# Optimization experiments

Hardware: AMD Instinct MI355X
Metric: run time of the kernel (lower is better)

## Reference

```python
import jax, jax.numpy as jnp
import numpy as np

B, S, D = 4, 1024, 1024
H, DK, DV = 16, 64, 64


def setup_inputs() -> dict:
    key = jax.random.key(0)
    ks = jax.random.split(key, 8)
    sc = 0.02
    return {
        "queries": jax.random.normal(ks[0], (B, S, D), jnp.float32),
        "keys": jax.random.normal(ks[1], (B, S, D), jnp.float32),
        "values": jax.random.normal(ks[2], (B, S, D), jnp.float32),
        "attn_bias": jax.random.normal(ks[3], (B, 1, S, S), jnp.float32),
        "Wq": jax.random.normal(ks[4], (H * DK, D), jnp.float32) * sc,
        "Wk": jax.random.normal(ks[5], (H * DK, D), jnp.float32) * sc,
        "Wv": jax.random.normal(ks[6], (H * DV, D), jnp.float32) * sc,
        "Wp": jax.random.normal(ks[7], (D, H * DV), jnp.float32) * sc,
    }


def reference(queries, keys, values, attn_bias, Wq, Wk, Wv, Wp):
    # Linear (no bias): x @ W.T, then split heads -> [B, H, S, d]
    q = (queries @ Wq.T).reshape(B, S, H, DK).transpose(0, 2, 1, 3)
    k = (keys @ Wk.T).reshape(B, S, H, DK).transpose(0, 2, 1, 3)
    v = (values @ Wv.T).reshape(B, S, H, DV).transpose(0, 2, 1, 3)
    # NOTE: original scales by d_model**-0.5, not d_key**-0.5
    scores = jnp.einsum("bhqd,bhkd->bhqk", q, k) * (D ** -0.5)
    scores = scores + attn_bias  # bias broadcasts over heads
    weights = jax.nn.softmax(scores, axis=-1)
    out = jnp.einsum("bhqk,bhkd->bhqd", weights, v)  # [B,H,S,DV]
    out = out.transpose(0, 2, 1, 3).reshape(B, S, H * DV)
    return out @ Wp.T
```

## Files before the change

kernel.cpp:

```cpp
#include <hip/hip_runtime.h>
#include <hip/hip_bf16.h>

typedef unsigned short u16;
typedef unsigned int u32;
typedef __attribute__((ext_vector_type(8))) short bf16x8;
typedef __attribute__((ext_vector_type(8))) u16 u16x8;
typedef __attribute__((ext_vector_type(4))) u16 u16x4;
typedef __attribute__((ext_vector_type(4))) u32 u32x4;
typedef __attribute__((ext_vector_type(4))) float f32x4;
typedef __attribute__((ext_vector_type(4))) _Float16 f16x4;
typedef __attribute__((ext_vector_type(8))) _Float16 f16x8;
typedef __attribute__((ext_vector_type(16))) float f32x16;

typedef const __attribute__((address_space(1))) void* gas1_t;
typedef __attribute__((address_space(3))) void* las3_t;

#define MFMA16(a,b,c) __builtin_amdgcn_mfma_f32_16x16x32_bf16((a),(b),(c),0,0,0)
#define MFMA32(a,b,c) __builtin_amdgcn_mfma_f32_32x32x16_bf16((a),(b),(c),0,0,0)

static constexpr int BB = 4, SS = 1024, DD = 1024, HH = 16;

static __device__ __forceinline__ u16 f2b(float x) {
  union { __hip_bfloat16 h; u16 u; } cv;
  cv.h = __float2bfloat16(x);
  return cv.u;
}
static __device__ __forceinline__ u32 pk2(float a, float b) {
  return (u32)f2b(a) | ((u32)f2b(b) << 16);
}
static __device__ __forceinline__ u32 cvtpk(float lo, float hi) {
  u32 r;
  asm("v_cvt_pk_bf16_f32 %0, %1, %2" : "=v"(r) : "v"(lo), "v"(hi));
  return r;
}

__global__ __launch_bounds__(256) void cvt_all(
    const float* __restrict__ wq_, const float* __restrict__ wk_, const float* __restrict__ wv_,
    const float* __restrict__ wp_, const float* __restrict__ bias,
    u16* __restrict__ wqb, u16* __restrict__ wkb, u16* __restrict__ wvb, u16* __restrict__ wpb,
    _Float16* __restrict__ bias16) {
  int bid = blockIdx.x;
  if (bid >= 4096) {
    int G = (bid - 4096) * 256 + threadIdx.x;
    int gi = G & 1023;
    int ctid = gi & 255, g = gi >> 8;
    int T = G >> 10;
    int kt = T & 15, qt = (T >> 4) & 7, b_ = T >> 7;
    int wq = ctid >> 6, hi = (ctid >> 5) & 1, ln = ctid & 31;
    int qrow = qt * 128 + wq * 32 + ln;
    int kbf = g >> 1, j = g & 1;
    int k0 = kt * 64 + kbf * 32 + j * 16 + hi * 4;
    const float* src = bias + (((size_t)(b_ * 1024 + qrow)) << 10) + k0;
    float4 lo = *(const float4*)(src);
    float4 up = *(const float4*)(src + 8);
    f16x8 r = { (_Float16)lo.x, (_Float16)lo.y, (_Float16)lo.z, (_Float16)lo.w,
                (_Float16)up.x, (_Float16)up.y, (_Float16)up.z, (_Float16)up.w };
    *(f16x8*)(bias16 + (((size_t)T) << 13) + g * 2048 + ctid * 8) = r;
    return;
  }
  const float* s; u16* d; int off;
  if      (bid < 1024) { s = wq_; d = wqb; off = bid; }
  else if (bid < 2048) { s = wk_; d = wkb; off = bid - 1024; }
  else if (bid < 3072) { s = wv_; d = wvb; off = bid - 2048; }
  else                 { s = wp_; d = wpb; off = bid - 3072; }
  int i = (off * 256 + threadIdx.x) * 4;
  float4 val = *(const float4*)(s + i);
  u16x4 r = { f2b(val.x), f2b(val.y), f2b(val.z), f2b(val.w) };
  *(u16x4*)(d + i) = r;
}

__global__ __launch_bounds__(512) void gemm_qkv(
    const float* __restrict__ Qf, const float* __restrict__ Kf, const float* __restrict__ Vf,
    const u16* __restrict__ Wbase, u16* __restrict__ Qb, u16* __restrict__ Kb,
    u16* __restrict__ Vtb) {
  const int z = blockIdx.z;
  const float* A = z == 0 ? Qf : (z == 1 ? Kf : Vf);
  const u16* W = Wbase + (size_t)z * (DD * DD);

  __shared__ __align__(16) float Af[128 * 64];
  __shared__ __align__(16) u16 Bs[128 * 64];

  const int tid = threadIdx.x;
  const int lane = tid & 63;
  const int wid = tid >> 6;
  const int g = lane >> 4;
  const int li = lane & 15;

  const int hw = blockIdx.x + (blockIdx.y << 3);
  const int L = ((hw & 7) << 5) + (hw >> 3);
  const int brow = (L >> 3) * 128;
  const int bcol = (L & 7) * 128;

  const int wr = (wid >> 1) * 32;
  const int wc = (wid & 1) * 64;

  const int arow = tid >> 4;
  const int apc = (tid & 15) ^ (arow & 15);
  const float* ga0 = A + (size_t)(brow + arow) * DD + apc * 4;

  const int srw = tid >> 3;
  const int spw = (tid & 7) ^ (srw & 7);
  const u16* gw0 = W + (size_t)(bcol + srw) * DD + spw * 8;

  f32x4 acc[2][4] = {};

  for (int k0 = 0; k0 < DD; k0 += 64) {
#pragma unroll
    for (int i = 0; i < 4; ++i)
      __builtin_amdgcn_global_load_lds((gas1_t)(const void*)(ga0 + (size_t)(i * 32) * DD + k0),
                                       (las3_t)(void*)(Af + (i * 32 + (wid << 2)) * 64), 16, 0, 0);
#pragma unroll
    for (int i = 0; i < 2; ++i)
      __builtin_amdgcn_global_load_lds((gas1_t)(const void*)(gw0 + (size_t)(i * 64) * DD + k0),
                                       (las3_t)(void*)(Bs + (i * 64 + (wid << 3)) * 64), 16, 0, 0);
    __syncthreads();

#pragma unroll
    for (int kk = 0; kk < 2; ++kk) {
      bf16x8 a[2], b[4];
#pragma unroll
      for (int m = 0; m < 2; ++m) {
        int row = wr + m * 16 + li;
        int gl = (2 * (kk * 4 + g)) ^ li;
        f32x4 alo = *(const f32x4*)&Af[row * 64 + gl * 4];
        f32x4 ahi = *(const f32x4*)&Af[row * 64 + (gl ^ 1) * 4];
        union { u32x4 u; bf16x8 v; } ac;
        ac.u = (u32x4){ cvtpk(alo[0], alo[1]), cvtpk(alo[2], alo[3]),
                        cvtpk(ahi[0], ahi[1]), cvtpk(ahi[2], ahi[3]) };
        a[m] = ac.v;
      }
#pragma unroll
      for (int n = 0; n < 4; ++n) {
        int row = wc + n * 16 + li;
        b[n] = *(const bf16x8*)&Bs[row * 64 + (((kk * 4 + g) ^ (li & 7)) << 3)];
      }
#pragma unroll
      for (int m = 0; m < 2; ++m)
#pragma unroll
        for (int n = 0; n < 4; ++n)
          acc[m][n] = MFMA16(a[m], b[n], acc[m][n]);
    }
    __syncthreads();
  }

  if (z == 2) {
#pragma unroll
    for (int m = 0; m < 2; ++m) {
#pragma unroll
      for (int n = 0; n < 4; ++n) {
        int c = bcol + wc + n * 16 + li;
        int h_ = c >> 6, dv = c & 63;
        int r0 = brow + wr + m * 16 + g * 4;
        int b_ = r0 >> 10, s0 = r0 & 1023;
        u16x4 val = { f2b(acc[m][n][0]), f2b(acc[m][n][1]),
                      f2b(acc[m][n][2]), f2b(acc[m][n][3]) };
        *(u16x4*)&Vtb[(size_t)((b_ * HH + h_) * 64 + dv) * SS + s0] = val;
      }
    }
  } else {
    u16* C = z == 0 ? Qb : Kb;
#pragma unroll
    for (int m = 0; m < 2; ++m)
#pragma unroll
      for (int n = 0; n < 4; ++n)
#pragma unroll
        for (int j = 0; j < 4; ++j) {
          int r = brow + wr + m * 16 + g * 4 + j;
          int c = bcol + wc + n * 16 + li;
          C[(size_t)r * DD + c] = f2b(acc[m][n][j]);
        }
  }
}

__global__ __launch_bounds__(512) void gemm_proj(
    const u16* __restrict__ A, const u16* __restrict__ W, float* __restrict__ C,
    int N, int K) {
  __shared__ __align__(16) u16 As[128 * 64];
  __shared__ __align__(16) u16 Bs[128 * 64];

  const int tid = threadIdx.x;
  const int lane = tid & 63;
  const int wid = tid >> 6;
  const int g = lane >> 4;
  const int li = lane & 15;

  const int hw = blockIdx.x + (blockIdx.y << 3);
  const int L = ((hw & 7) << 5) + (hw >> 3);
  const int brow = (L >> 3) * 128;
  const int bcol = (L & 7) * 128;

  const int wr = (wid >> 1) * 32;
  const int wc = (wid & 1) * 64;

  const int srow = tid >> 3;
  const int schunk = (tid & 7) ^ (srow & 7);
  const u16* ga0 = A + (size_t)(brow + srow) * K + schunk * 8;
  const u16* gw0 = W + (size_t)(bcol + srow) * K + schunk * 8;

  f32x4 acc[2][4] = {};

  for (int k0 = 0; k0 < K; k0 += 64) {
#pragma unroll
    for (int i = 0; i < 2; ++i) {
      __builtin_amdgcn_global_load_lds((gas1_t)(const void*)(ga0 + (size_t)(i * 64) * K + k0),
                                       (las3_t)(void*)(As + (i * 64 + (wid << 3)) * 64), 16, 0, 0);
      __builtin_amdgcn_global_load_lds((gas1_t)(const void*)(gw0 + (size_t)(i * 64) * K + k0),
                                       (las3_t)(void*)(Bs + (i * 64 + (wid << 3)) * 64), 16, 0, 0);
    }
    __syncthreads();

#pragma unroll
    for (int kk = 0; kk < 2; ++kk) {
      bf16x8 a[2], b[4];
#pragma unroll
      for (int m = 0; m < 2; ++m) {
        int row = wr + m * 16 + li;
        a[m] = *(const bf16x8*)&As[row * 64 + (((kk * 4 + g) ^ (li & 7)) << 3)];
      }
#pragma unroll
      for (int n = 0; n < 4; ++n) {
        int row = wc + n * 16 + li;
        b[n] = *(const bf16x8*)&Bs[row * 64 + (((kk * 4 + g) ^ (li & 7)) << 3)];
      }
#pragma unroll
      for (int m = 0; m < 2; ++m)
#pragma unroll
        for (int n = 0; n < 4; ++n)
          acc[m][n] = MFMA16(a[m], b[n], acc[m][n]);
    }
    __syncthreads();
  }

#pragma unroll
  for (int m = 0; m < 2; ++m)
#pragma unroll
    for (int n = 0; n < 4; ++n)
#pragma unroll
      for (int j = 0; j < 4; ++j) {
        int r = brow + wr + m * 16 + g * 4 + j;
        int c = bcol + wc + n * 16 + li;
        C[(size_t)r * N + c] = acc[m][n][j];
      }
}

__global__ __launch_bounds__(256) void attn_kernel(
    const u16* __restrict__ Q, const u16* __restrict__ K, const u16* __restrict__ Vt,
    const _Float16* __restrict__ bias16, u16* __restrict__ O) {
  __shared__ __align__(16) u16 kbuf[2][64 * 64];
  __shared__ __align__(16) u16 vbuf[2][64 * 64];

  const int tid = threadIdx.x;
  const int lane = tid & 63;
  const int wq = tid >> 6;
  const int hi = lane >> 5;
  const int ln = lane & 31;
  const u32 swz = (u32)(ln & 7) << 4;

  const int flat = blockIdx.x + (blockIdx.y << 3) + (blockIdx.z << 7);
  const int L = ((flat & 7) << 6) | (flat >> 3);
  const int qt = L & 7, h = (L >> 3) & 15, b = L >> 7;
  const int q0 = qt * 128;
  const int qrow = q0 + wq * 32 + ln;

  bf16x8 qf[4];
  {
    const u16* qp = Q + (size_t)(b * SS + qrow) * DD + h * 64 + hi * 8;
#pragma unroll
    for (int d = 0; d < 4; ++d) qf[d] = *(const bf16x8*)(qp + d * 16);
  }

  const int srow = (lane >> 3);
  const int spc = ((lane & 7) ^ srow) * 8;
  const u16* kgl = K + (size_t)(b * SS + wq * 16 + srow) * DD + h * 64 + spc;
  const u16* vgl = Vt + (size_t)((b * HH + h) * 64 + wq * 16 + srow) * SS + spc;

  const _Float16* btile = bias16 + (((size_t)(b * 8 + qt) * 16) << 13) + tid * 8;

  {
    char* kd = (char*)kbuf[0] + wq * 2048;
    char* vd = (char*)vbuf[0] + wq * 2048;
#pragma unroll
    for (int j = 0; j < 2; ++j) {
      __builtin_amdgcn_global_load_lds((gas1_t)(const void*)(kgl + (size_t)(j * 8) * DD),
                                       (las3_t)(void*)(kd + j * 1024), 16, 0, 0);
      __builtin_amdgcn_global_load_lds((gas1_t)(const void*)(vgl + (size_t)(j * 8) * SS),
                                       (las3_t)(void*)(vd + j * 1024), 16, 0, 0);
    }
  }
  f16x8 bbr[4], bbn[4];
#pragma unroll
  for (int g = 0; g < 4; ++g)
    bbr[g] = *(const f16x8*)(btile + g * 2048);
  __syncthreads();

  f32x16 o0 = {}, o1 = {};
  float m = -1e30f, lsum = 0.f;
  int cur = 0;

  for (int kt = 0; kt < 16; ++kt) {
    if (kt < 15) {
      char* kd = (char*)kbuf[cur ^ 1] + wq * 2048;
      char* vd = (char*)vbuf[cur ^ 1] + wq * 2048;
      const size_t k1 = (size_t)(kt + 1) * 64;
#pragma unroll
      for (int j = 0; j < 2; ++j) {
        __builtin_amdgcn_global_load_lds((gas1_t)(const void*)(kgl + (k1 + j * 8) * DD),
                                         (las3_t)(void*)(kd + j * 1024), 16, 0, 0);
        __builtin_amdgcn_global_load_lds((gas1_t)(const void*)(vgl + (size_t)(j * 8) * SS + k1),
                                         (las3_t)(void*)(vd + j * 1024), 16, 0, 0);
      }
      const _Float16* bt = btile + ((size_t)(kt + 1) << 13);
#pragma unroll
      for (int g = 0; g < 4; ++g)
        bbn[g] = *(const f16x8*)(bt + g * 2048);
    }

    const char* kb_base = (const char*)kbuf[cur];
    f32x16 s[2];
#pragma unroll
    for (int kb = 0; kb < 2; ++kb) {
      f32x16 acc = {};
#pragma unroll
      for (int d = 0; d < 4; ++d) {
        bf16x8 kf = *(const bf16x8*)(kb_base + (kb * 32 + ln) * 128 + (((u32)(d * 32 + hi * 16)) ^ swz));
        acc = MFMA32(kf, qf[d], acc);
      }
      s[kb] = acc;
    }

#pragma unroll
    for (int g = 0; g < 4; ++g) {
      const int kb = g >> 1, rq0 = (g & 1) * 2;
#pragma unroll
      for (int e = 0; e < 8; ++e)
        s[kb][(rq0 + (e >> 2)) * 4 + (e & 3)] =
            fmaf(s[kb][(rq0 + (e >> 2)) * 4 + (e & 3)], 0.03125f, (float)bbr[g][e]);
    }

    float mt = -1e30f;
#pragma unroll
    for (int r = 0; r < 16; ++r) { mt = fmaxf(mt, s[0][r]); mt = fmaxf(mt, s[1][r]); }
    mt = fmaxf(mt, __shfl_xor(mt, 32));

    bool resc = false;
    float fsc = 1.f;
    if (kt == 0) {
      m = mt;
    } else if (__any(mt > m + 8.f)) {
      float mn = fmaxf(m, mt);
      fsc = __expf(m - mn);
      m = mn;
      resc = true;
    }

    float rs = 0.f;
    u32 wv[2][8];
#pragma unroll
    for (int kb = 0; kb < 2; ++kb)
#pragma unroll
      for (int t = 0; t < 8; ++t) {
        float p0 = __expf(s[kb][2 * t] - m);
        float p1 = __expf(s[kb][2 * t + 1] - m);
        rs += p0 + p1;
        wv[kb][t] = pk2(p0, p1);
      }
    rs += __shfl_xor(rs, 32);
    lsum = lsum * fsc + rs;

    if (resc) {
#pragma unroll
      for (int j = 0; j < 16; ++j) {
        float fv = __shfl(fsc, (j & 3) + 8 * (j >> 2) + 4 * hi);
        o0[j] *= fv; o1[j] *= fv;
      }
    }

    const char* vb_base = (const char*)vbuf[cur];
#pragma unroll
    for (int ks = 0; ks < 4; ++ks) {
      const int kb = ks >> 1, i0 = (ks & 1) * 4;
      u32 sA = hi ? wv[kb][i0 + 0] : wv[kb][i0 + 2];
      u32 sB = hi ? wv[kb][i0 + 1] : wv[kb][i0 + 3];
      u32 rA = (u32)__shfl_xor((int)sA, 32);
      u32 rB = (u32)__shfl_xor((int)sB, 32);
      u32 e0 = hi ? rA : wv[kb][i0 + 0];
      u32 e1 = hi ? rB : wv[kb][i0 + 1];
      u32 e2 = hi ? wv[kb][i0 + 2] : rA;
      u32 e3 = hi ? wv[kb][i0 + 3] : rB;
      union { u32x4 u; bf16x8 v; } pc;
      pc.u = (u32x4){e0, e1, e2, e3};
      bf16x8 pa = pc.v;
#pragma unroll
      for (int nv = 0; nv < 2; ++nv) {
        bf16x8 vf = *(const bf16x8*)(vb_base + (nv * 32 + ln) * 128 + (((u32)(ks * 32 + hi * 16)) ^ swz));
        if (nv == 0) o0 = MFMA32(pa, vf, o0);
        else         o1 = MFMA32(pa, vf, o1);
      }
    }

    if (kt < 15) {
      __syncthreads();
      cur ^= 1;
#pragma unroll
      for (int g = 0; g < 4; ++g) bbr[g] = bbn[g];
    }
  }

  float inv = 1.0f / lsum;
#pragma unroll
  for (int j = 0; j < 16; ++j) {
    float iv = __shfl(inv, (j & 3) + 8 * (j >> 2) + 4 * hi);
    int q = q0 + wq * 32 + (j & 3) + 8 * (j >> 2) + 4 * hi;
    u16* op = O + (size_t)(b * SS + q) * DD + h * 64 + ln;
    op[0]  = f2b(o0[j] * iv);
    op[32] = f2b(o1[j] * iv);
  }
}

extern "C" void kernel_launch(void* const* d_in, const int* in_sizes, int n_in,
                              void* d_out, int out_size, void* d_ws, size_t ws_size,
                              hipStream_t stream) {
  const float* queries = (const float*)d_in[0];
  const float* keys    = (const float*)d_in[1];
  const float* values  = (const float*)d_in[2];
  const float* bias    = (const float*)d_in[3];
  const float* Wq      = (const float*)d_in[4];
  const float* Wk      = (const float*)d_in[5];
  const float* Wv      = (const float*)d_in[6];
  const float* Wp      = (const float*)d_in[7];
  float* out = (float*)d_out;

  char* ws = (char*)d_ws;
  const size_t MB = 1024 * 1024;
  u16* wqb = (u16*)(ws + 24 * MB);
  u16* wkb = (u16*)(ws + 26 * MB);
  u16* wvb = (u16*)(ws + 28 * MB);
  u16* wpb = (u16*)(ws + 30 * MB);
  u16* Qb  = (u16*)(ws + 32 * MB);
  u16* Kb  = (u16*)(ws + 40 * MB);
  _Float16* bias16 = (_Float16*)(ws + 48 * MB);
  u16* Vtb = (u16*)(ws + 56 * MB);
  u16* Ob  = (u16*)(ws + 0 * MB);

  cvt_all<<<dim3(6144), dim3(256), 0, stream>>>(
      Wq, Wk, Wv, Wp, bias, wqb, wkb, wvb, wpb, bias16);

  gemm_qkv<<<dim3(8, 32, 3), dim3(512), 0, stream>>>(
      queries, keys, values, wqb, Qb, Kb, Vtb);

  attn_kernel<<<dim3(8, 16, 4), dim3(256), 0, stream>>>(Qb, Kb, Vtb, bias16, Ob);

  gemm_proj<<<dim3(8, 32, 1), dim3(512), 0, stream>>>(Ob, wpb, out, DD, DD);
}
```

Baseline: 119.4 us.

## Register-prefetch fp32 A tiles and store bf16 to LDS in QKV GEMM

The QKV projection GEMM no longer copies fp32 activation tiles directly into LDS and converts them at every MFMA operand read. Each thread now loads the next fp32 A slice into registers one iteration ahead, converts it to bf16 once, and writes a swizzled bf16 tile to LDS. This halves the A tile's LDS footprint and removes repeated conversion work in the inner loop. In exchange it uses more registers and issues ordinary global loads instead of async global-to-LDS transfers.

```diff
diff --git a/kernel.cpp b/kernel.cpp
--- a/kernel.cpp
+++ b/kernel.cpp
@@ -6,6 +6,7 @@
 typedef __attribute__((ext_vector_type(8))) short bf16x8;
 typedef __attribute__((ext_vector_type(8))) u16 u16x8;
 typedef __attribute__((ext_vector_type(4))) u16 u16x4;
+typedef __attribute__((ext_vector_type(2))) u32 u32x2;
 typedef __attribute__((ext_vector_type(4))) u32 u32x4;
 typedef __attribute__((ext_vector_type(4))) float f32x4;
 typedef __attribute__((ext_vector_type(4))) _Float16 f16x4;
@@ -77,7 +78,7 @@
   const float* A = z == 0 ? Qf : (z == 1 ? Kf : Vf);
   const u16* W = Wbase + (size_t)z * (DD * DD);
 
-  __shared__ __align__(16) float Af[128 * 64];
+  __shared__ __align__(16) u16 As[128 * 64];
   __shared__ __align__(16) u16 Bs[128 * 64];
 
   const int tid = threadIdx.x;
@@ -95,8 +96,9 @@
   const int wc = (wid & 1) * 64;
 
   const int arow = tid >> 4;
-  const int apc = (tid & 15) ^ (arow & 15);
-  const float* ga0 = A + (size_t)(brow + arow) * DD + apc * 4;
+  const int ag = tid & 15;
+  const float* ga0 = A + (size_t)(brow + arow) * DD + ag * 4;
+  const u32 awb = (u32)((((ag >> 1) ^ (arow & 7)) << 4) + ((ag & 1) << 3));
 
   const int srw = tid >> 3;
   const int spw = (tid & 7) ^ (srw & 7);
@@ -104,15 +106,33 @@
 
   f32x4 acc[2][4] = {};
 
+  f32x4 ar0 = *(const f32x4*)(ga0 + (size_t)(0 * 32) * DD);
+  f32x4 ar1 = *(const f32x4*)(ga0 + (size_t)(1 * 32) * DD);
+  f32x4 ar2 = *(const f32x4*)(ga0 + (size_t)(2 * 32) * DD);
+  f32x4 ar3 = *(const f32x4*)(ga0 + (size_t)(3 * 32) * DD);
+
   for (int k0 = 0; k0 < DD; k0 += 64) {
-#pragma unroll
-    for (int i = 0; i < 4; ++i)
-      __builtin_amdgcn_global_load_lds((gas1_t)(const void*)(ga0 + (size_t)(i * 32) * DD + k0),
-                                       (las3_t)(void*)(Af + (i * 32 + (wid << 2)) * 64), 16, 0, 0);
 #pragma unroll
     for (int i = 0; i < 2; ++i)
       __builtin_amdgcn_global_load_lds((gas1_t)(const void*)(gw0 + (size_t)(i * 64) * DD + k0),
                                        (las3_t)(void*)(Bs + (i * 64 + (wid << 3)) * 64), 16, 0, 0);
+    {
+      u32x2 w0 = { cvtpk(ar0[0], ar0[1]), cvtpk(ar0[2], ar0[3]) };
+      u32x2 w1 = { cvtpk(ar1[0], ar1[1]), cvtpk(ar1[2], ar1[3]) };
+      u32x2 w2 = { cvtpk(ar2[0], ar2[1]), cvtpk(ar2[2], ar2[3]) };
+      u32x2 w3 = { cvtpk(ar3[0], ar3[1]), cvtpk(ar3[2], ar3[3]) };
+      char* ab = (char*)As + arow * 128 + awb;
+      *(u32x2*)(ab + 0 * 32 * 128) = w0;
+      *(u32x2*)(ab + 1 * 32 * 128) = w1;
+      *(u32x2*)(ab + 2 * 32 * 128) = w2;
+      *(u32x2*)(ab + 3 * 32 * 128) = w3;
+    }
+    if (k0 < DD - 64) {
+      ar0 = *(const f32x4*)(ga0 + (size_t)(0 * 32) * DD + k0 + 64);
+      ar1 = *(const f32x4*)(ga0 + (size_t)(1 * 32) * DD + k0 + 64);
+      ar2 = *(const f32x4*)(ga0 + (size_t)(2 * 32) * DD + k0 + 64);
+      ar3 = *(const f32x4*)(ga0 + (size_t)(3 * 32) * DD + k0 + 64);
+    }
     __syncthreads();
 
 #pragma unroll
@@ -121,13 +141,7 @@
 #pragma unroll
       for (int m = 0; m < 2; ++m) {
         int row = wr + m * 16 + li;
-        int gl = (2 * (kk * 4 + g)) ^ li;
-        f32x4 alo = *(const f32x4*)&Af[row * 64 + gl * 4];
-        f32x4 ahi = *(const f32x4*)&Af[row * 64 + (gl ^ 1) * 4];
-        union { u32x4 u; bf16x8 v; } ac;
-        ac.u = (u32x4){ cvtpk(alo[0], alo[1]), cvtpk(alo[2], alo[3]),
-                        cvtpk(ahi[0], ahi[1]), cvtpk(ahi[2], ahi[3]) };
-        a[m] = ac.v;
+        a[m] = *(const bf16x8*)&As[row * 64 + (((kk * 4 + g) ^ (li & 7)) << 3)];
       }
 #pragma unroll
       for (int n = 0; n < 4; ++n) {
```

New measurement: 112.0 us, median of 3. 1.07x faster.

## Double-buffer QKV GEMM with register-prefetched fp32 A converted to bf16 LDS

Applied to the files above, without the earlier changes.

Restructures the QKV projection GEMM main loop into a two-stage software pipeline. LDS is double-buffered for both operands. The fp32 activation tile is prefetched into registers two K-steps ahead and converted to bf16 once before being written to a swizzled LDS buffer, rather than being loaded as fp32 via direct-to-LDS and converted on every fragment read. This removes one barrier per iteration and shrinks LDS traffic for A, at the cost of more registers for the staging arrays and synchronous global loads.

```diff
diff --git a/kernel.cpp b/kernel.cpp
--- a/kernel.cpp
+++ b/kernel.cpp
@@ -6,6 +6,7 @@
 typedef __attribute__((ext_vector_type(8))) short bf16x8;
 typedef __attribute__((ext_vector_type(8))) u16 u16x8;
 typedef __attribute__((ext_vector_type(4))) u16 u16x4;
+typedef __attribute__((ext_vector_type(2))) u32 u32x2;
 typedef __attribute__((ext_vector_type(4))) u32 u32x4;
 typedef __attribute__((ext_vector_type(4))) float f32x4;
 typedef __attribute__((ext_vector_type(4))) _Float16 f16x4;
@@ -77,8 +78,8 @@
   const float* A = z == 0 ? Qf : (z == 1 ? Kf : Vf);
   const u16* W = Wbase + (size_t)z * (DD * DD);
 
-  __shared__ __align__(16) float Af[128 * 64];
-  __shared__ __align__(16) u16 Bs[128 * 64];
+  __shared__ __align__(16) u16 As[2][128 * 64];
+  __shared__ __align__(16) u16 Bs[2][128 * 64];
 
   const int tid = threadIdx.x;
   const int lane = tid & 63;
@@ -95,44 +96,50 @@
   const int wc = (wid & 1) * 64;
 
   const int arow = tid >> 4;
-  const int apc = (tid & 15) ^ (arow & 15);
-  const float* ga0 = A + (size_t)(brow + arow) * DD + apc * 4;
+  const int ag = tid & 15;
+  const float* ga0 = A + (size_t)(brow + arow) * DD + ag * 4;
+  const u32 awb = (u32)((((ag >> 1) ^ (arow & 7)) << 4) + ((ag & 1) << 3));
 
   const int srw = tid >> 3;
   const int spw = (tid & 7) ^ (srw & 7);
   const u16* gw0 = W + (size_t)(bcol + srw) * DD + spw * 8;
 
   f32x4 acc[2][4] = {};
-
-  for (int k0 = 0; k0 < DD; k0 += 64) {
+  f32x4 sa[4], sb[4];
+
+  auto loadA = [&](f32x4* S, int kt) {
 #pragma unroll
     for (int i = 0; i < 4; ++i)
-      __builtin_amdgcn_global_load_lds((gas1_t)(const void*)(ga0 + (size_t)(i * 32) * DD + k0),
-                                       (las3_t)(void*)(Af + (i * 32 + (wid << 2)) * 64), 16, 0, 0);
+      S[i] = *(const f32x4*)(ga0 + (size_t)(i * 32) * DD + kt * 64);
+  };
+  auto stageA = [&](const f32x4* S, u16* dst) {
+    char* ab = (char*)dst + arow * 128 + awb;
+#pragma unroll
+    for (int i = 0; i < 4; ++i) {
+      u32x2 w = { cvtpk(S[i][0], S[i][1]), cvtpk(S[i][2], S[i][3]) };
+      *(u32x2*)(ab + i * 32 * 128) = w;
+    }
+  };
+  auto stageW = [&](int kt, u16* dst) {
 #pragma unroll
     for (int i = 0; i < 2; ++i)
-      __builtin_amdgcn_global_load_lds((gas1_t)(const void*)(gw0 + (size_t)(i * 64) * DD + k0),
-                                       (las3_t)(void*)(Bs + (i * 64 + (wid << 3)) * 64), 16, 0, 0);
-    __syncthreads();
-
+      __builtin_amdgcn_global_load_lds(
+          (gas1_t)(const void*)(gw0 + (size_t)(i * 64) * DD + kt * 64),
+          (las3_t)(void*)(dst + (i * 64 + (wid << 3)) * 64), 16, 0, 0);
+  };
+  auto compute = [&](const u16* Asb, const u16* Bsb) {
 #pragma unroll
     for (int kk = 0; kk < 2; ++kk) {
       bf16x8 a[2], b[4];
 #pragma unroll
       for (int m = 0; m < 2; ++m) {
         int row = wr + m * 16 + li;
-        int gl = (2 * (kk * 4 + g)) ^ li;
-        f32x4 alo = *(const f32x4*)&Af[row * 64 + gl * 4];
-        f32x4 ahi = *(const f32x4*)&Af[row * 64 + (gl ^ 1) * 4];
-        union { u32x4 u; bf16x8 v; } ac;
-        ac.u = (u32x4){ cvtpk(alo[0], alo[1]), cvtpk(alo[2], alo[3]),
-                        cvtpk(ahi[0], ahi[1]), cvtpk(ahi[2], ahi[3]) };
-        a[m] = ac.v;
+        a[m] = *(const bf16x8*)&Asb[row * 64 + (((kk * 4 + g) ^ (li & 7)) << 3)];
       }
 #pragma unroll
       for (int n = 0; n < 4; ++n) {
         int row = wc + n * 16 + li;
-        b[n] = *(const bf16x8*)&Bs[row * 64 + (((kk * 4 + g) ^ (li & 7)) << 3)];
+        b[n] = *(const bf16x8*)&Bsb[row * 64 + (((kk * 4 + g) ^ (li & 7)) << 3)];
       }
 #pragma unroll
       for (int m = 0; m < 2; ++m)
@@ -140,7 +147,35 @@
         for (int n = 0; n < 4; ++n)
           acc[m][n] = MFMA16(a[m], b[n], acc[m][n]);
     }
-    __syncthreads();
+  };
+
+  loadA(sa, 0);
+  stageW(0, Bs[0]);
+  stageA(sa, As[0]);
+  loadA(sb, 1);
+  __syncthreads();
+
+  for (int k2 = 0; k2 < 16; k2 += 2) {
+    {
+      const int k = k2;
+      if (k < 15) {
+        stageW(k + 1, Bs[1]);
+        if (k < 14) loadA(sa, k + 2);
+        stageA(sb, As[1]);
+      }
+      compute(As[0], Bs[0]);
+      if (k < 15) __syncthreads();
+    }
+    {
+      const int k = k2 + 1;
+      if (k < 15) {
+        stageW(k + 1, Bs[0]);
+        if (k < 14) loadA(sb, k + 2);
+        stageA(sa, As[0]);
+      }
+      compute(As[1], Bs[1]);
+      if (k < 15) __syncthreads();
+    }
   }
 
   if (z == 2) {
```

Measured after the change: 115.4 us. -3.4%, faster.
